# Performance work log

Measured on AMD Instinct MI355X. Metric: run time of the kernel, lower is better.

Reference implementation:

```python
import jax, jax.numpy as jnp
import numpy as np
from jax.lax.linalg import triangular_solve

B, T, D = 4, 2048, 1024
H, HD = 16, 64
K_OPS, R = 4, 48
POWER_K = 2
RIDGE_EPS = 1e-4
LN_EPS = 1e-5


def setup_inputs() -> dict:
    key = jax.random.key(0)
    ks = jax.random.split(key, 8)
    s = 1.0 / np.sqrt(D)
    return {
        "hidden_states": jax.random.normal(ks[0], (B, T, D), dtype=jnp.float32),
        "W_K_ops": jax.random.normal(ks[1], (K_OPS, D, H * R), dtype=jnp.float32) * s,
        "W_Q_ops": jax.random.normal(ks[2], (K_OPS, D, H * R), dtype=jnp.float32) * s,
        "W_V": jax.random.normal(ks[3], (D, H * HD), dtype=jnp.float32) * s,
        "W_O": jax.random.normal(ks[4], (H * HD, D), dtype=jnp.float32) * (1.0 / np.sqrt(H * HD)),
        "ln_gamma": jnp.ones((D,), dtype=jnp.float32),
        "ln_beta": jnp.zeros((D,), dtype=jnp.float32),
        "gate_alphas": jnp.zeros((K_OPS,), dtype=jnp.float32),
        "gate_alpha": jnp.zeros((1,), dtype=jnp.float32),
        "log_ridges": jnp.full((K_OPS,), np.log(RIDGE_EPS), dtype=jnp.float32),
        "log_gammas": jnp.zeros((K_OPS,), dtype=jnp.float32),
        "prefix_len": T // 2,
    }


def _layer_norm(x, g, b):
    mu = jnp.mean(x, axis=-1, keepdims=True)
    var = jnp.var(x, axis=-1, keepdims=True)
    return (x - mu) * jax.lax.rsqrt(var + LN_EPS) * g + b


def _solve_lower(L, rhs, transpose=False):
    # batched solve of L x = rhs (or L^T x = rhs), L lower-triangular [.., r, r]
    return triangular_solve(L, rhs, left_side=True, lower=True, transpose_a=transpose)


def reference(hidden_states, W_K_ops, W_Q_ops, W_V, W_O, ln_gamma, ln_beta,
              gate_alphas, gate_alpha, log_ridges, log_gammas, prefix_len):
    Bsz, Tlen, _ = hidden_states.shape
    pl = max(1, min(int(prefix_len), Tlen - 1))
    normed = _layer_norm(hidden_states, ln_gamma, ln_beta)
    # values: [B, H, T, HD]
    values = (normed @ W_V).reshape(Bsz, Tlen, H, HD).transpose(0, 2, 1, 3)
    eye_r = jnp.eye(R, dtype=hidden_states.dtype)
    acc = jnp.zeros((Bsz, H, Tlen, HD), dtype=hidden_states.dtype)
    for k in range(K_OPS):
        ridge = jnp.exp(log_ridges[k])
        gamma = jnp.exp(log_gammas[k])
        gate_k = jax.nn.sigmoid(gate_alphas[k])
        keys = (normed @ W_K_ops[k]).reshape(Bsz, Tlen, H, R).transpose(0, 2, 1, 3)    # [B,H,T,R]
        queries = (normed @ W_Q_ops[k]).reshape(Bsz, Tlen, H, R).transpose(0, 2, 1, 3)  # [B,H,T,R]
        pk = keys[:, :, :pl, :]   # prefix keys [B,H,pl,R]
        # Gram and cross-covariance (rank-R, batched over B*H)
        G = jnp.einsum('bhlr,bhls->bhrs', pk, pk) + ridge * eye_r
        M = jnp.einsum('bhlr,bhls->bhrs', pk[:, :, 1:, :], pk[:, :, :-1, :])
        Lc = jnp.linalg.cholesky(G)                         # [B,H,R,R] lower
        U = _solve_lower(Lc, M)
        V = _solve_lower(Lc, jnp.swapaxes(U, -1, -2))
        A_w = jnp.swapaxes(V, -1, -2)                       # Koopman operator [B,H,R,R]
        # spectral-norm scaling
        sigma_max = jnp.linalg.svd(A_w, compute_uv=False)[..., 0][..., None, None]
        sigma_max = jnp.maximum(sigma_max, 1e-8)
        scale = jnp.minimum(gamma, 1.0) / jnp.maximum(sigma_max, 1.0)
        A_w = A_w * scale
        # value readout B_v = C_v G^{-1}
        pv = values[:, :, :pl, :]
        C_v = jnp.einsum('bhld,bhlr->bhdr', pv, pk)          # [B,H,HD,R]
        Y_T = _solve_lower(Lc, jnp.swapaxes(C_v, -1, -2))
        Bv_T = _solve_lower(Lc, Y_T, transpose=True)
        B_v = jnp.swapaxes(Bv_T, -1, -2)                     # [B,H,HD,R]
        # whitened queries + power iteration
        q_t = jnp.swapaxes(queries, -1, -2)                  # [B,H,R,T]
        w_f = _solve_lower(Lc, q_t)
        for _ in range(POWER_K):
            w_f = A_w @ w_f
        z_hat = Lc @ w_f                                     # [B,H,R,T]
        out_k = jnp.swapaxes(B_v @ z_hat, -1, -2)            # [B,H,T,HD]
        acc = acc + gate_k * out_k
    out = acc.transpose(0, 2, 1, 3).reshape(Bsz, Tlen, H * HD) @ W_O
    return jax.nn.sigmoid(gate_alpha) * out
```

## Files before the change

kernel.cpp:

```cpp
#include <hip/hip_runtime.h>
#include <math.h>

typedef unsigned short u16;
typedef __attribute__((ext_vector_type(8))) short bf16x8;
typedef __attribute__((ext_vector_type(4))) float f32x4;

#define BSZ 4
#define TLEN 2048
#define DDIM 1024
#define NH 16
#define HDIM 64
#define NKOPS 4
#define RDIM 48
#define HR 768
#define HHD 1024
#define NALL 4096
#define LNEPS 1e-5f
#define GSPLIT 16
#define SST 52

#define AS1 __attribute__((address_space(1)))
#define AS3 __attribute__((address_space(3)))

static __device__ __forceinline__ void gload16(const u16* g, u16* l) {
    __builtin_amdgcn_global_load_lds((const AS1 unsigned int*)g, (AS3 unsigned int*)l, 16, 0, 0);
}

static __device__ __forceinline__ int clamp_pl(int p) {
    if (p < 1) p = 1;
    if (p > TLEN - 1) p = TLEN - 1;
    return p;
}

static __device__ __forceinline__ u16 f2bf(float x) {
    unsigned u = __float_as_uint(x);
    return (u16)((u + 0x7FFFu + ((u >> 16) & 1u)) >> 16);
}
static __device__ __forceinline__ float bf2f(u16 h) {
    return __uint_as_float(((unsigned)h) << 16);
}

static __device__ __forceinline__ float dot48(const float* __restrict__ a,
                                              const float* __restrict__ b) {
    float s0 = 0.f, s1 = 0.f, s2 = 0.f, s3 = 0.f;
#pragma unroll
    for (int m = 0; m < 12; ++m) {
        float4 av = *(const float4*)(a + m * 4);
        float4 bv = *(const float4*)(b + m * 4);
        s0 += av.x * bv.x; s1 += av.y * bv.y;
        s2 += av.z * bv.z; s3 += av.w * bv.w;
    }
    return (s0 + s1) + (s2 + s3);
}

static __device__ __forceinline__ void mm48_3x3(const float* __restrict__ Lb,
                                                const float* __restrict__ Rb,
                                                int i0, int j0, float acc[3][3]) {
#pragma unroll
    for (int r = 0; r < 3; ++r)
#pragma unroll
        for (int c = 0; c < 3; ++c) acc[r][c] = 0.f;
#pragma unroll 4
    for (int m = 0; m < 12; ++m) {
        float4 a0 = *(const float4*)(Lb + (i0 + 0) * SST + m * 4);
        float4 a1 = *(const float4*)(Lb + (i0 + 1) * SST + m * 4);
        float4 a2 = *(const float4*)(Lb + (i0 + 2) * SST + m * 4);
        float4 b0 = *(const float4*)(Rb + (j0 + 0) * SST + m * 4);
        float4 b1 = *(const float4*)(Rb + (j0 + 1) * SST + m * 4);
        float4 b2 = *(const float4*)(Rb + (j0 + 2) * SST + m * 4);
        acc[0][0] += a0.x * b0.x + a0.y * b0.y + a0.z * b0.z + a0.w * b0.w;
        acc[0][1] += a0.x * b1.x + a0.y * b1.y + a0.z * b1.z + a0.w * b1.w;
        acc[0][2] += a0.x * b2.x + a0.y * b2.y + a0.z * b2.z + a0.w * b2.w;
        acc[1][0] += a1.x * b0.x + a1.y * b0.y + a1.z * b0.z + a1.w * b0.w;
        acc[1][1] += a1.x * b1.x + a1.y * b1.y + a1.z * b1.z + a1.w * b1.w;
        acc[1][2] += a1.x * b2.x + a1.y * b2.y + a1.z * b2.z + a1.w * b2.w;
        acc[2][0] += a2.x * b0.x + a2.y * b0.y + a2.z * b0.z + a2.w * b0.w;
        acc[2][1] += a2.x * b1.x + a2.y * b1.y + a2.z * b1.z + a2.w * b1.w;
        acc[2][2] += a2.x * b2.x + a2.y * b2.y + a2.z * b2.z + a2.w * b2.w;
    }
}

#define WB() __builtin_amdgcn_wave_barrier()

__global__ __launch_bounds__(256) void ln_kernel(const float* __restrict__ hs,
                                                 const float* __restrict__ g,
                                                 const float* __restrict__ b,
                                                 u16* __restrict__ nh,
                                                 u16* __restrict__ nl)
{
    int row = blockIdx.x;
    int tid = threadIdx.x;
    const float* x = hs + (size_t)row * DDIM;
    float4 v = ((const float4*)x)[tid];
    float s  = v.x + v.y + v.z + v.w;
    float ss = v.x*v.x + v.y*v.y + v.z*v.z + v.w*v.w;
    for (int off = 32; off > 0; off >>= 1) {
        s  += __shfl_down(s, off);
        ss += __shfl_down(ss, off);
    }
    __shared__ float rs[4], rss[4], st[2];
    int wid = tid >> 6, lane = tid & 63;
    if (lane == 0) { rs[wid] = s; rss[wid] = ss; }
    __syncthreads();
    if (tid == 0) {
        float S  = rs[0] + rs[1] + rs[2] + rs[3];
        float SS = rss[0] + rss[1] + rss[2] + rss[3];
        float mu = S / (float)DDIM;
        float var = SS / (float)DDIM - mu * mu;
        st[0] = mu;
        st[1] = rsqrtf(var + LNEPS);
    }
    __syncthreads();
    float mu = st[0], rstd = st[1];
    float4 gv = ((const float4*)g)[tid];
    float4 bv = ((const float4*)b)[tid];
    float o[4];
    o[0] = (v.x - mu) * rstd * gv.x + bv.x;
    o[1] = (v.y - mu) * rstd * gv.y + bv.y;
    o[2] = (v.z - mu) * rstd * gv.z + bv.z;
    o[3] = (v.w - mu) * rstd * gv.w + bv.w;
    u16 h[4], l[4];
#pragma unroll
    for (int i = 0; i < 4; ++i) {
        h[i] = f2bf(o[i]);
        l[i] = f2bf(o[i] - bf2f(h[i]));
    }
    uint2 ph, pl2;
    ph.x = (unsigned)h[0] | ((unsigned)h[1] << 16);
    ph.y = (unsigned)h[2] | ((unsigned)h[3] << 16);
    pl2.x = (unsigned)l[0] | ((unsigned)l[1] << 16);
    pl2.y = (unsigned)l[2] | ((unsigned)l[3] << 16);
    *(uint2*)(nh + (size_t)row * DDIM + tid * 4) = ph;
    *(uint2*)(nl + (size_t)row * DDIM + tid * 4) = pl2;
}

__global__ __launch_bounds__(256) void transcvt(const float* __restrict__ in,
                                                u16* __restrict__ oh,
                                                u16* __restrict__ ol,
                                                int R, int C)
{
    __shared__ float t[32][33];
    int bx = blockIdx.x, by = blockIdx.y;
    int tx = threadIdx.x & 31, ty = threadIdx.x >> 5;
#pragma unroll
    for (int j = 0; j < 4; ++j)
        t[ty + j * 8][tx] = in[(size_t)(by * 32 + ty + j * 8) * C + bx * 32 + tx];
    __syncthreads();
#pragma unroll
    for (int j = 0; j < 4; ++j) {
        float v = t[tx][ty + j * 8];
        u16 h = f2bf(v);
        size_t o = (size_t)(bx * 32 + ty + j * 8) * R + by * 32 + tx;
        oh[o] = h;
        ol[o] = f2bf(v - bf2f(h));
    }
}

__global__ __launch_bounds__(256) void transcvt_wk(const float* __restrict__ WK,
                                                   u16* __restrict__ oh,
                                                   u16* __restrict__ ol)
{
    __shared__ float t[32][33];
    int bx = blockIdx.x, by = blockIdx.y, k = blockIdx.z;
    const float* in = WK + (size_t)k * DDIM * HR;
    u16* ohk = oh + (size_t)k * (HR * DDIM);
    u16* olk = ol + (size_t)k * (HR * DDIM);
    int tx = threadIdx.x & 31, ty = threadIdx.x >> 5;
#pragma unroll
    for (int j = 0; j < 4; ++j)
        t[ty + j * 8][tx] = in[(size_t)(by * 32 + ty + j * 8) * HR + bx * 32 + tx];
    __syncthreads();
#pragma unroll
    for (int j = 0; j < 4; ++j) {
        float v = t[tx][ty + j * 8];
        u16 h = f2bf(v);
        size_t o = (size_t)(bx * 32 + ty + j * 8) * DDIM + by * 32 + tx;
        ohk[o] = h;
        olk[o] = f2bf(v - bf2f(h));
    }
}

template<int OMODE>
__global__ __launch_bounds__(256) void gemm_mfma(
    const u16* __restrict__ Ah, const u16* __restrict__ Al, long sAz,
    const u16* __restrict__ Bth, const u16* __restrict__ Btl, long sBz,
    float* __restrict__ C, u16* __restrict__ Oh, u16* __restrict__ Ol, long sCz,
    int M, int N, int K,
    const int* __restrict__ pl_ptr, const float* __restrict__ gate_ptr)
{
    int z = blockIdx.z;
    int m0 = blockIdx.y * 128, n0 = blockIdx.x * 128;
    if (pl_ptr) {
        int p = clamp_pl(pl_ptr[0]);
        if (m0 >= (p < M ? p : M)) return;
    }
    Ah  += (size_t)z * sAz;  Al  += (size_t)z * sAz;
    Bth += (size_t)z * sBz;  Btl += (size_t)z * sBz;

    __shared__ u16 As[2][128][32];
    __shared__ u16 Bs[2][128][32];

    int tid = threadIdx.x;
    int wid = tid >> 6, ln = tid & 63;
    int wm = (wid >> 1) * 64, wn = (wid & 1) * 64;
    int r16 = ln & 15, kg = ln >> 4;

    int rb = wid * 32;
    int lr = ln >> 2;
    int sl = ln & 3;
    int koff = (sl ^ (((rb + lr) >> 1) & 3)) * 8;

    const u16* gA0h = Ah  + (size_t)(m0 + rb + lr) * K + koff;
    const u16* gA1h = gA0h + (size_t)16 * K;
    const u16* gA0l = Al  + (size_t)(m0 + rb + lr) * K + koff;
    const u16* gA1l = gA0l + (size_t)16 * K;
    const u16* gB0h = Bth + (size_t)(n0 + rb + lr) * K + koff;
    const u16* gB1h = gB0h + (size_t)16 * K;
    const u16* gB0l = Btl + (size_t)(n0 + rb + lr) * K + koff;
    const u16* gB1l = gB0l + (size_t)16 * K;

    u16* lA0h = &As[0][rb][0];      u16* lA1h = &As[0][rb + 16][0];
    u16* lA0l = &As[1][rb][0];      u16* lA1l = &As[1][rb + 16][0];
    u16* lB0h = &Bs[0][rb][0];      u16* lB1h = &Bs[0][rb + 16][0];
    u16* lB0l = &Bs[1][rb][0];      u16* lB1l = &Bs[1][rb + 16][0];

    f32x4 acc[4][4];
#pragma unroll
    for (int mt = 0; mt < 4; ++mt)
#pragma unroll
        for (int nt = 0; nt < 4; ++nt)
            acc[mt][nt] = (f32x4){0.f, 0.f, 0.f, 0.f};

    for (int k0 = 0; k0 < K; k0 += 32) {
        __syncthreads();
        gload16(gA0h, lA0h);  gload16(gA1h, lA1h);
        gload16(gA0l, lA0l);  gload16(gA1l, lA1l);
        gload16(gB0h, lB0h);  gload16(gB1h, lB1h);
        gload16(gB0l, lB0l);  gload16(gB1l, lB1l);
        gA0h += 32; gA1h += 32; gA0l += 32; gA1l += 32;
        gB0h += 32; gB1h += 32; gB0l += 32; gB1l += 32;
        __syncthreads();

        bf16x8 bhf[4], blf[4];
#pragma unroll
        for (int nt = 0; nt < 4; ++nt) {
            int r = wn + nt * 16 + r16;
            int s = (kg ^ ((r >> 1) & 3)) * 8;
            bhf[nt] = *(const bf16x8*)&Bs[0][r][s];
            blf[nt] = *(const bf16x8*)&Bs[1][r][s];
        }
#pragma unroll
        for (int mt = 0; mt < 4; ++mt) {
            int r = wm + mt * 16 + r16;
            int s = (kg ^ ((r >> 1) & 3)) * 8;
            bf16x8 ah = *(const bf16x8*)&As[0][r][s];
            bf16x8 al = *(const bf16x8*)&As[1][r][s];
#pragma unroll
            for (int nt = 0; nt < 4; ++nt) {
                acc[mt][nt] = __builtin_amdgcn_mfma_f32_16x16x32_bf16(ah, bhf[nt], acc[mt][nt], 0, 0, 0);
                acc[mt][nt] = __builtin_amdgcn_mfma_f32_16x16x32_bf16(ah, blf[nt], acc[mt][nt], 0, 0, 0);
                acc[mt][nt] = __builtin_amdgcn_mfma_f32_16x16x32_bf16(al, bhf[nt], acc[mt][nt], 0, 0, 0);
            }
        }
    }

    int orow0 = m0 + wm + kg * 4;
    int ocol0 = n0 + wn + r16;
    if (OMODE == 0) {
        float scale = 1.0f;
        if (gate_ptr) scale = 1.0f / (1.0f + expf(-gate_ptr[0]));
        float* Cz = C + (size_t)z * sCz;
#pragma unroll
        for (int mt = 0; mt < 4; ++mt)
#pragma unroll
            for (int nt = 0; nt < 4; ++nt)
#pragma unroll
                for (int j = 0; j < 4; ++j)
                    Cz[(size_t)(orow0 + mt * 16 + j) * N + ocol0 + nt * 16] = acc[mt][nt][j] * scale;
    } else {
        u16* Ohz = Oh + (size_t)z * sCz;
        u16* Olz = Ol + (size_t)z * sCz;
#pragma unroll
        for (int mt = 0; mt < 4; ++mt)
#pragma unroll
            for (int nt = 0; nt < 4; ++nt)
#pragma unroll
                for (int j = 0; j < 4; ++j) {
                    float v = acc[mt][nt][j];
                    u16 h = f2bf(v);
                    size_t o = (size_t)(orow0 + mt * 16 + j) * N + ocol0 + nt * 16;
                    Ohz[o] = h;
                    Olz[o] = f2bf(v - bf2f(h));
                }
    }
}

__global__ __launch_bounds__(256) void gram_kernel(const float* __restrict__ Kp,
                                                   const float* __restrict__ Vp,
                                                   float* __restrict__ Gpart,
                                                   float* __restrict__ Mpart,
                                                   float* __restrict__ Cpart,
                                                   const int* __restrict__ pl_ptr)
{
    int h = blockIdx.x, b = blockIdx.y, sp = blockIdx.z;
    int pl = clamp_pl(pl_ptr[0]);
    __shared__ float pks[65][48];
    __shared__ float pvs[64][64];
    int tid = threadIdx.x;
    int tx = tid & 15, ty = tid >> 4;
    float gacc[3][3] = {}, macc[3][3] = {}, cacc[4][3] = {};
    const float* Kbase = Kp + (size_t)b * TLEN * HR + h * RDIM;
    const float* Vbase = Vp + (size_t)b * TLEN * HHD + h * HDIM;
    const float4 z4 = make_float4(0.f, 0.f, 0.f, 0.f);

    for (int c0 = sp * 64; c0 < pl; c0 += GSPLIT * 64) {
        for (int idx = tid; idx < 65 * 12; idx += 256) {
            int rr = idx / 12, c4 = idx % 12;
            int tg = c0 + rr;
            *(float4*)&pks[rr][c4 * 4] =
                (tg < pl) ? *(const float4*)&Kbase[(size_t)tg * HR + c4 * 4] : z4;
        }
        for (int idx = tid; idx < 64 * 16; idx += 256) {
            int rr = idx >> 4, c4 = idx & 15;
            int tg = c0 + rr;
            *(float4*)&pvs[rr][c4 * 4] =
                (tg < pl) ? *(const float4*)&Vbase[(size_t)tg * HHD + c4 * 4] : z4;
        }
        __syncthreads();
        float cura[3], curb[3];
#pragma unroll
        for (int i = 0; i < 3; ++i) {
            cura[i] = pks[0][tx * 3 + i];
            curb[i] = pks[0][ty * 3 + i];
        }
#pragma unroll 2
        for (int l = 0; l < 64; ++l) {
            float nxta[3], nxtb[3];
#pragma unroll
            for (int i = 0; i < 3; ++i) {
                nxta[i] = pks[l + 1][tx * 3 + i];
                nxtb[i] = pks[l + 1][ty * 3 + i];
            }
            float4 v4 = *(const float4*)&pvs[l][ty * 4];
            float vv[4] = { v4.x, v4.y, v4.z, v4.w };
#pragma unroll
            for (int i = 0; i < 3; ++i)
#pragma unroll
                for (int j = 0; j < 3; ++j) {
                    gacc[i][j] += cura[i] * curb[j];
                    macc[i][j] += nxta[i] * curb[j];
                }
#pragma unroll
            for (int j = 0; j < 4; ++j)
#pragma unroll
                for (int i = 0; i < 3; ++i)
                    cacc[j][i] += vv[j] * cura[i];
#pragma unroll
            for (int i = 0; i < 3; ++i) { cura[i] = nxta[i]; curb[i] = nxtb[i]; }
        }
        __syncthreads();
    }
    size_t pbase = (size_t)sp * (BSZ * NH) + b * NH + h;
    float* Gp = Gpart + pbase * 2304;
    float* Mp = Mpart + pbase * 2304;
    float* Cp = Cpart + pbase * 3072;
#pragma unroll
    for (int i = 0; i < 3; ++i)
#pragma unroll
        for (int j = 0; j < 3; ++j) {
            Gp[(tx * 3 + i) * 48 + (ty * 3 + j)] = gacc[i][j];
            Mp[(tx * 3 + i) * 48 + (ty * 3 + j)] = macc[i][j];
        }
#pragma unroll
    for (int j = 0; j < 4; ++j)
#pragma unroll
        for (int i = 0; i < 3; ++i)
            Cp[(ty * 4 + j) * 48 + (tx * 3 + i)] = cacc[j][i];
}

__global__ __launch_bounds__(256) void gram_all(const float* __restrict__ Call,
                                                float* __restrict__ Gpart,
                                                float* __restrict__ Mpart,
                                                float* __restrict__ Cpart,
                                                const int* __restrict__ pl_ptr)
{
    int h = blockIdx.x, b = blockIdx.y, zz = blockIdx.z;
    int k = zz >> 2, sp = zz & 3;
    int pl = clamp_pl(pl_ptr[0]);
    __shared__ float pks[65][48];
    __shared__ float pvs[64][64];
    int tid = threadIdx.x;
    int tx = tid & 15, ty = tid >> 4;
    float gacc[3][3] = {}, macc[3][3] = {}, cacc[4][3] = {};
    const float* Kbase = Call + (size_t)b * TLEN * NALL + (HHD + k * HR) + h * RDIM;
    const float* Vbase = Call + (size_t)b * TLEN * NALL + h * HDIM;
    const float4 z4 = make_float4(0.f, 0.f, 0.f, 0.f);

    for (int c0 = sp * 64; c0 < pl; c0 += 4 * 64) {
        for (int idx = tid; idx < 65 * 12; idx += 256) {
            int rr = idx / 12, c4 = idx % 12;
            int tg = c0 + rr;
            *(float4*)&pks[rr][c4 * 4] =
                (tg < pl) ? *(const float4*)&Kbase[(size_t)tg * NALL + c4 * 4] : z4;
        }
        for (int idx = tid; idx < 64 * 16; idx += 256) {
            int rr = idx >> 4, c4 = idx & 15;
            int tg = c0 + rr;
            *(float4*)&pvs[rr][c4 * 4] =
                (tg < pl) ? *(const float4*)&Vbase[(size_t)tg * NALL + c4 * 4] : z4;
        }
        __syncthreads();
        float cura[3], curb[3];
#pragma unroll
        for (int i = 0; i < 3; ++i) {
            cura[i] = pks[0][tx * 3 + i];
            curb[i] = pks[0][ty * 3 + i];
        }
#pragma unroll 2
        for (int l = 0; l < 64; ++l) {
            float nxta[3], nxtb[3];
#pragma unroll
            for (int i = 0; i < 3; ++i) {
                nxta[i] = pks[l + 1][tx * 3 + i];
                nxtb[i] = pks[l + 1][ty * 3 + i];
            }
            float4 v4 = *(const float4*)&pvs[l][ty * 4];
            float vv[4] = { v4.x, v4.y, v4.z, v4.w };
#pragma unroll
            for (int i = 0; i < 3; ++i)
#pragma unroll
                for (int j = 0; j < 3; ++j) {
                    gacc[i][j] += cura[i] * curb[j];
                    macc[i][j] += nxta[i] * curb[j];
                }
#pragma unroll
            for (int j = 0; j < 4; ++j)
#pragma unroll
                for (int i = 0; i < 3; ++i)
                    cacc[j][i] += vv[j] * cura[i];
#pragma unroll
            for (int i = 0; i < 3; ++i) { cura[i] = nxta[i]; curb[i] = nxtb[i]; }
        }
        __syncthreads();
    }
    size_t pbase = (size_t)zz * (BSZ * NH) + b * NH + h;
    float* Gp = Gpart + pbase * 2304;
    float* Mp = Mpart + pbase * 2304;
    float* Cp = Cpart + pbase * 3072;
#pragma unroll
    for (int i = 0; i < 3; ++i)
#pragma unroll
        for (int j = 0; j < 3; ++j) {
            Gp[(tx * 3 + i) * 48 + (ty * 3 + j)] = gacc[i][j];
            Mp[(tx * 3 + i) * 48 + (ty * 3 + j)] = macc[i][j];
        }
#pragma unroll
    for (int j = 0; j < 4; ++j)
#pragma unroll
        for (int i = 0; i < 3; ++i)
            Cp[(ty * 4 + j) * 48 + (tx * 3 + i)] = cacc[j][i];
}

__global__ __launch_bounds__(256) void gram_reduce(const float* __restrict__ Gpart,
                                                   const float* __restrict__ Mpart,
                                                   const float* __restrict__ Cpart,
                                                   float* __restrict__ Gb,
                                                   float* __restrict__ Mb,
                                                   float* __restrict__ Cb,
                                                   int k)
{
    int p = blockIdx.x;
    size_t ob = ((size_t)k * (BSZ * NH) + p);
    for (int idx = threadIdx.x; idx < 2304; idx += 256) {
        float sg = 0.f, sm = 0.f;
#pragma unroll
        for (int sp = 0; sp < GSPLIT; ++sp) {
            size_t pb = ((size_t)sp * (BSZ * NH) + p);
            sg += Gpart[pb * 2304 + idx];
            sm += Mpart[pb * 2304 + idx];
        }
        Gb[ob * 2304 + idx] = sg;
        Mb[ob * 2304 + idx] = sm;
    }
    for (int idx = threadIdx.x; idx < 3072; idx += 256) {
        float sc = 0.f;
#pragma unroll
        for (int sp = 0; sp < GSPLIT; ++sp)
            sc += Cpart[((size_t)sp * (BSZ * NH) + p) * 3072 + idx];
        Cb[ob * 3072 + idx] = sc;
    }
}

__global__ __launch_bounds__(256) void gram_reduce_all(const float* __restrict__ Gpart,
                                                       const float* __restrict__ Mpart,
                                                       const float* __restrict__ Cpart,
                                                       float* __restrict__ Gb,
                                                       float* __restrict__ Mb,
                                                       float* __restrict__ Cb)
{
    int blk = blockIdx.x;
    int k = blk >> 6, p = blk & 63;
    size_t ob = (size_t)blk;
    for (int idx = threadIdx.x; idx < 2304; idx += 256) {
        float sg = 0.f, sm = 0.f;
#pragma unroll
        for (int sp = 0; sp < 4; ++sp) {
            size_t pb = ((size_t)(k * 4 + sp) * (BSZ * NH) + p);
            sg += Gpart[pb * 2304 + idx];
            sm += Mpart[pb * 2304 + idx];
        }
        Gb[ob * 2304 + idx] = sg;
        Mb[ob * 2304 + idx] = sm;
    }
    for (int idx = threadIdx.x; idx < 3072; idx += 256) {
        float sc = 0.f;
#pragma unroll
        for (int sp = 0; sp < 4; ++sp)
            sc += Cpart[((size_t)(k * 4 + sp) * (BSZ * NH) + p) * 3072 + idx];
        Cb[ob * 3072 + idx] = sc;
    }
}

__global__ __launch_bounds__(256) void solver_kernel(const float* __restrict__ Gb,
                                                     const float* __restrict__ Mb,
                                                     const float* __restrict__ Cb,
                                                     float* __restrict__ Fb,
                                                     const float* __restrict__ log_ridges,
                                                     const float* __restrict__ log_gammas)
{
    int blk = blockIdx.x;
    int k = blk / (BSZ * NH);
    int tid = threadIdx.x;
    int ti = tid >> 4, tj = tid & 15;
    int i0 = ti * 3, j0 = tj * 3;

    __shared__ float A [48 * SST];
    __shared__ float Hs[48 * SST];
    __shared__ float Mm[48 * SST];
    __shared__ float Pm[48 * SST];
    __shared__ float Pt[48 * SST];
    __shared__ float pvb[4][SST];

    size_t base = (size_t)blk;
    const float* Gp = Gb + base * 2304;
    const float* Mp = Mb + base * 2304;
    const float* Cp = Cb + base * 3072;
    float ridge = expf(log_ridges[k]);

    for (int idx = tid; idx < 2304; idx += 256) {
        int i = idx / 48, j = idx % 48;
        A [i * SST + j] = Gp[idx] + ((i == j) ? ridge : 0.f);
        Hs[i * SST + j] = (i == j) ? 1.f : 0.f;
        Mm[i * SST + j] = Mp[idx];
    }
    __syncthreads();

    for (int p = 0; p < 48; ++p) {
        int p4 = p >> 2;
        float pr = 1.0f / fmaxf(A[p * SST + p], 1e-30f);
        int c4a = p4 + 1;
        int nA4 = 11 - p4;
        int nb  = 3 - (p & 3);
        for (int q = tid; q < 576; q += 256) {
            int i = q / 12, c = q % 12;
            if (i == p) continue;
            float f = A[i * SST + p] * pr;
            if (c < nA4) {
                int c4 = c4a + c;
                float4 prw = *(const float4*)&A[p * SST + c4 * 4];
                float4* d = (float4*)&A[i * SST + c4 * 4];
                float4 v = *d;
                v.x -= f * prw.x; v.y -= f * prw.y;
                v.z -= f * prw.z; v.w -= f * prw.w;
                *d = v;
            } else {
                int c4 = c - nA4;
                float4 prw = *(const float4*)&Hs[p * SST + c4 * 4];
                float4* d = (float4*)&Hs[i * SST + c4 * 4];
                float4 v = *d;
                v.x -= f * prw.x; v.y -= f * prw.y;
                v.z -= f * prw.z; v.w -= f * prw.w;
                *d = v;
            }
        }
        if (nb) {
            for (int i = tid; i < 48; i += 256) {
                if (i == p) continue;
                float f = A[i * SST + p] * pr;
                for (int c = p + 1; c < 4 * c4a; ++c)
                    A[i * SST + c] -= f * A[p * SST + c];
            }
        }
        __syncthreads();
    }
    for (int idx = tid; idx < 2304; idx += 256) {
        int i = idx / 48, j = idx % 48;
        Hs[i * SST + j] /= fmaxf(A[i * SST + i], 1e-30f);
    }
    __syncthreads();
    for (int idx = tid; idx < 2304; idx += 256) {
        int i = idx / 48, j = idx % 48;
        A[j * SST + i] = Mm[i * SST + j];
    }
    __syncthreads();
    {
        float acc[3][3];
        mm48_3x3(Hs, A, i0, j0, acc);
#pragma unroll
        for (int r = 0; r < 3; ++r)
#pragma unroll
            for (int c = 0; c < 3; ++c) {
                Pm[(i0 + r) * SST + j0 + c] = acc[r][c];
                Pt[(j0 + c) * SST + i0 + r] = acc[r][c];
            }
    }
    __syncthreads();
    {
        float acc[3][3];
        mm48_3x3(Hs, Mm, i0, j0, acc);
        __syncthreads();
#pragma unroll
        for (int r = 0; r < 3; ++r)
#pragma unroll
            for (int c = 0; c < 3; ++c)
                A[(i0 + r) * SST + j0 + c] = acc[r][c];
    }
    __syncthreads();
    {
        float acc[3][3];
        mm48_3x3(A, Pt, i0, j0, acc);
        __syncthreads();
#pragma unroll
        for (int r = 0; r < 3; ++r)
#pragma unroll
            for (int c = 0; c < 3; ++c) {
                Mm[(i0 + r) * SST + j0 + c] = acc[r][c];
                A [(j0 + c) * SST + i0 + r] = acc[r][c];
            }
    }
    __syncthreads();
    {
        float acc[3][3];
        mm48_3x3(Mm, A, i0, j0, acc);
#pragma unroll
        for (int r = 0; r < 3; ++r)
#pragma unroll
            for (int c = 0; c < 3; ++c)
                Pt[(i0 + r) * SST + j0 + c] = acc[r][c];
    }
    __syncthreads();
    for (int idx = tid; idx < 2304; idx += 256) {
        int i = idx / 48, j = idx % 48;
        A[j * SST + i] = Pt[i * SST + j];
    }
    __syncthreads();
    {
        float acc[3][3];
        mm48_3x3(Pt, A, i0, j0, acc);
        __syncthreads();
#pragma unroll
        for (int r = 0; r < 3; ++r)
#pragma unroll
            for (int c = 0; c < 3; ++c)
                Mm[(i0 + r) * SST + j0 + c] = acc[r][c];
    }
    __syncthreads();

    int ln = tid & 63, w = tid >> 6;
    float* pv = pvb[w];
    if (ln < 48) pv[ln] = ((float)((ln * 2654435761u) & 0xFFFF)) / 65536.0f + 0.5f;
    WB();
    float lam = 0.f;
    for (int it = 0; it < 25; ++it) {
        float z = 0.f;
        if (ln < 48) z = dot48(&Mm[ln * SST], pv);
        if (it == 24) {
            float nn = z * z;
            for (int off = 1; off < 64; off <<= 1) nn += __shfl_xor(nn, off);
            lam = sqrtf(nn);
            break;
        }
        if ((it & 1) == 1) {
            float nn = z * z;
            for (int off = 1; off < 64; off <<= 1) nn += __shfl_xor(nn, off);
            z *= rsqrtf(fmaxf(nn, 1e-30f));
        }
        WB();
        if (ln < 48) pv[ln] = z;
        WB();
    }
    float sigma = sqrtf(sqrtf(sqrtf(fmaxf(lam, 0.f))));
    float gamma = expf(log_gammas[k]);
    float scl = fminf(gamma, 1.f) / fmaxf(fmaxf(sigma, 1e-8f), 1.f);
    float s2 = scl * scl;

    {
        float acc[3][3];
        mm48_3x3(Pm, Hs, i0, j0, acc);
        __syncthreads();
#pragma unroll
        for (int r = 0; r < 3; ++r)
#pragma unroll
            for (int c = 0; c < 3; ++c)
                A[(j0 + c) * SST + i0 + r] = acc[r][c];
    }
    __syncthreads();
    {
        float acc[3][3];
        mm48_3x3(Pm, A, i0, j0, acc);
        __syncthreads();
#pragma unroll
        for (int r = 0; r < 3; ++r)
#pragma unroll
            for (int c = 0; c < 3; ++c)
                Pt[(j0 + c) * SST + i0 + r] = s2 * acc[r][c];
    }
    __syncthreads();
    for (int idx = tid; idx < 3072; idx += 256) {
        int row = idx / 48, col = idx % 48;
        float v = Cp[idx];
        if (row < 48) Mm[row * SST + col] = v;
        else          A [(row - 48) * SST + col] = v;
    }
    __syncthreads();
    {
        int fi0 = ti * 4, fj0 = tj * 3;
        const float* crow0 = (fi0 < 48) ? &Mm[fi0 * SST] : &A[(fi0 - 48) * SST];
        float acc[4][3];
#pragma unroll
        for (int r = 0; r < 4; ++r)
#pragma unroll
            for (int c = 0; c < 3; ++c) acc[r][c] = 0.f;
#pragma unroll 4
        for (int m = 0; m < 12; ++m) {
            float4 a0 = *(const float4*)(crow0 + 0 * SST + m * 4);
            float4 a1 = *(const float4*)(crow0 + 1 * SST + m * 4);
            float4 a2 = *(const float4*)(crow0 + 2 * SST + m * 4);
            float4 a3 = *(const float4*)(crow0 + 3 * SST + m * 4);
            float4 b0 = *(const float4*)(&Pt[(fj0 + 0) * SST] + m * 4);
            float4 b1 = *(const float4*)(&Pt[(fj0 + 1) * SST] + m * 4);
            float4 b2 = *(const float4*)(&Pt[(fj0 + 2) * SST] + m * 4);
            acc[0][0] += a0.x*b0.x + a0.y*b0.y + a0.z*b0.z + a0.w*b0.w;
            acc[0][1] += a0.x*b1.x + a0.y*b1.y + a0.z*b1.z + a0.w*b1.w;
            acc[0][2] += a0.x*b2.x + a0.y*b2.y + a0.z*b2.z + a0.w*b2.w;
            acc[1][0] += a1.x*b0.x + a1.y*b0.y + a1.z*b0.z + a1.w*b0.w;
            acc[1][1] += a1.x*b1.x + a1.y*b1.y + a1.z*b1.z + a1.w*b1.w;
            acc[1][2] += a1.x*b2.x + a1.y*b2.y + a1.z*b2.z + a1.w*b2.w;
            acc[2][0] += a2.x*b0.x + a2.y*b0.y + a2.z*b0.z + a2.w*b0.w;
            acc[2][1] += a2.x*b1.x + a2.y*b1.y + a2.z*b1.z + a2.w*b1.w;
            acc[2][2] += a2.x*b2.x + a2.y*b2.y + a2.z*b2.z + a2.w*b2.w;
            acc[3][0] += a3.x*b0.x + a3.y*b0.y + a3.z*b0.z + a3.w*b0.w;
            acc[3][1] += a3.x*b1.x + a3.y*b1.y + a3.z*b1.z + a3.w*b1.w;
            acc[3][2] += a3.x*b2.x + a3.y*b2.y + a3.z*b2.z + a3.w*b2.w;
        }
#pragma unroll
        for (int r = 0; r < 4; ++r)
#pragma unroll
            for (int c = 0; c < 3; ++c)
                Fb[base * 3072 + (size_t)(fi0 + r) * 48 + fj0 + c] = acc[r][c];
    }
}

__global__ __launch_bounds__(256) void wcmb_kernel(const float* __restrict__ WQ,
                                                   const float* __restrict__ Fb,
                                                   const float* __restrict__ gate_alphas,
                                                   u16* __restrict__ Wh,
                                                   u16* __restrict__ Wl)
{
    int dt = blockIdx.x;
    int h = blockIdx.y, b = blockIdx.z;
    __shared__ float wq[64][49];
    __shared__ float fs[64][49];
    int tid = threadIdx.x;
    int tx = tid & 15, ty = tid >> 4;
    float acc[4][4] = {};
    for (int k = 0; k < NKOPS; ++k) {
        float gate = 1.0f / (1.0f + expf(-gate_alphas[k]));
        for (int idx = tid; idx < 64 * 48; idx += 256) {
            int rr = idx / 48, cc = idx % 48;
            wq[rr][cc] = WQ[((size_t)k * DDIM + dt * 64 + rr) * HR + h * RDIM + cc];
            fs[rr][cc] = gate * Fb[(((size_t)k * BSZ + b) * NH + h) * 3072 + idx];
        }
        __syncthreads();
        for (int r = 0; r < 48; ++r) {
            float a[4], bb[4];
#pragma unroll
            for (int i = 0; i < 4; ++i) { a[i] = wq[tx * 4 + i][r]; bb[i] = fs[ty * 4 + i][r]; }
#pragma unroll
            for (int i = 0; i < 4; ++i)
#pragma unroll
                for (int j = 0; j < 4; ++j)
                    acc[i][j] += a[i] * bb[j];
        }
        __syncthreads();
    }
#pragma unroll
    for (int i = 0; i < 4; ++i)
#pragma unroll
        for (int j = 0; j < 4; ++j) {
            size_t o = ((size_t)b * DDIM + dt * 64 + tx * 4 + i) * HHD + h * HDIM + ty * 4 + j;
            float v = acc[i][j];
            u16 hh = f2bf(v);
            Wh[o] = hh;
            Wl[o] = f2bf(v - bf2f(hh));
        }
}

extern "C" void kernel_launch(void* const* d_in, const int* in_sizes, int n_in,
                              void* d_out, int out_size, void* d_ws, size_t ws_size,
                              hipStream_t stream)
{
    const float* hs          = (const float*)d_in[0];
    const float* WK          = (const float*)d_in[1];
    const float* WQ          = (const float*)d_in[2];
    const float* WV          = (const float*)d_in[3];
    const float* WO          = (const float*)d_in[4];
    const float* ln_g        = (const float*)d_in[5];
    const float* ln_b        = (const float*)d_in[6];
    const float* gate_alphas = (const float*)d_in[7];
    const float* gate_alpha  = (const float*)d_in[8];
    const float* log_ridges  = (const float*)d_in[9];
    const float* log_gammas  = (const float*)d_in[10];
    const int*   pl_ptr      = (const int*)d_in[11];
    float* out = (float*)d_out;
    float* wsf = (float*)d_ws;

    float* Gpart = out;
    float* Mpart = out + 2359296;
    float* Cpart = out + 4718592;

    const size_t BIG_NEED = (size_t)(12582912 + 33554432) * 4;

    if (ws_size >= BIG_NEED) {
        u16* n_hi    = (u16*)(wsf + 0);
        u16* n_lo    = (u16*)(wsf + 4194304);
        u16* Wall_h  = (u16*)(wsf + 8388608);
        u16* Wall_l  = (u16*)(wsf + 10485760);
        u16* WVt_h   = Wall_h;
        u16* WVt_l   = Wall_l;
        u16* WKt_ah  = Wall_h + (size_t)HHD * DDIM;
        u16* WKt_al  = Wall_l + (size_t)HHD * DDIM;
        float* Call  = wsf + 12582912;
        float* Gb    = Call;
        float* Mb    = Call + 589824;
        float* Cb    = Call + 1179648;
        u16* WOt_h   = (u16*)(Call + 2097152);
        u16* WOt_l   = (u16*)(Call + 2621440);
        float* Fb    = Call + 3145728;
        u16* Wcmb_h  = (u16*)(Call + 4194304);
        u16* Wcmb_l  = (u16*)(Call + 6291456);
        u16* Wfint_h = (u16*)(Call + 8388608);
        u16* Wfint_l = (u16*)(Call + 10485760);

        ln_kernel<<<BSZ * TLEN, 256, 0, stream>>>(hs, ln_g, ln_b, n_hi, n_lo);
        transcvt<<<dim3(HHD / 32, DDIM / 32), 256, 0, stream>>>(WV, WVt_h, WVt_l, DDIM, HHD);
        transcvt_wk<<<dim3(HR / 32, DDIM / 32, NKOPS), 256, 0, stream>>>(WK, WKt_ah, WKt_al);

        gemm_mfma<0><<<dim3(NALL / 128, TLEN / 128, BSZ), 256, 0, stream>>>(
            n_hi, n_lo, (long)TLEN * DDIM, Wall_h, Wall_l, 0,
            Call, nullptr, nullptr, (long)TLEN * NALL,
            TLEN, NALL, DDIM, pl_ptr, nullptr);

        gram_all<<<dim3(NH, BSZ, 16), 256, 0, stream>>>(Call, Gpart, Mpart, Cpart, pl_ptr);
        gram_reduce_all<<<NKOPS * BSZ * NH, 256, 0, stream>>>(Gpart, Mpart, Cpart, Gb, Mb, Cb);

        transcvt<<<dim3(DDIM / 32, HHD / 32), 256, 0, stream>>>(WO, WOt_h, WOt_l, HHD, DDIM);

        solver_kernel<<<NKOPS * BSZ * NH, 256, 0, stream>>>(Gb, Mb, Cb, Fb, log_ridges, log_gammas);
        wcmb_kernel<<<dim3(DDIM / 64, NH, BSZ), 256, 0, stream>>>(WQ, Fb, gate_alphas, Wcmb_h, Wcmb_l);

        gemm_mfma<1><<<dim3(DDIM / 128, DDIM / 128, BSZ), 256, 0, stream>>>(
            WOt_h, WOt_l, 0, Wcmb_h, Wcmb_l, (long)DDIM * HHD,
            nullptr, Wfint_h, Wfint_l, (long)DDIM * DDIM,
            DDIM, DDIM, HHD, nullptr, nullptr);

        gemm_mfma<0><<<dim3(DDIM / 128, TLEN / 128, BSZ), 256, 0, stream>>>(
            n_hi, n_lo, (long)TLEN * DDIM, Wfint_h, Wfint_l, (long)DDIM * DDIM,
            out, nullptr, nullptr, (long)TLEN * DDIM,
            TLEN, DDIM, DDIM, nullptr, gate_alpha);
        return;
    }

    u16* n_hi    = (u16*)(wsf + 0);
    u16* n_lo    = (u16*)(wsf + 4194304);
    u16* WVt_h   = (u16*)(wsf + 8388608);
    u16* WVt_l   = (u16*)(wsf + 8912896);
    u16* WKt_ah  = (u16*)(wsf + 9437184);
    u16* WKt_al  = (u16*)(wsf + 11010048);
    float* Vp    = wsf + 12582912;
    float* Kp    = wsf + 20971520;
    float* Gb    = wsf + 27262976;
    float* Mb    = wsf + 27852800;
    float* Cb    = wsf + 28442624;
    u16* Wcmb_h  = (u16*)Vp;
    u16* Wcmb_l  = (u16*)(Vp + 2097152);
    u16* Wfint_h = (u16*)(Vp + 4194304);
    u16* Wfint_l = (u16*)(Vp + 6291456);
    u16* WOt_h   = (u16*)Kp;
    u16* WOt_l   = (u16*)(Kp + 524288);
    float* Fb    = Kp + 1048576;

    ln_kernel<<<BSZ * TLEN, 256, 0, stream>>>(hs, ln_g, ln_b, n_hi, n_lo);
    transcvt_wk<<<dim3(HR / 32, DDIM / 32, NKOPS), 256, 0, stream>>>(WK, WKt_ah, WKt_al);
    transcvt<<<dim3(HHD / 32, DDIM / 32), 256, 0, stream>>>(WV, WVt_h, WVt_l, DDIM, HHD);

    gemm_mfma<0><<<dim3(HHD / 128, TLEN / 128, BSZ), 256, 0, stream>>>(
        n_hi, n_lo, (long)TLEN * DDIM, WVt_h, WVt_l, 0,
        Vp, nullptr, nullptr, (long)TLEN * HHD,
        TLEN, HHD, DDIM, pl_ptr, nullptr);

    for (int k = 0; k < NKOPS; ++k) {
        gemm_mfma<0><<<dim3(HR / 128, TLEN / 128, BSZ), 256, 0, stream>>>(
            n_hi, n_lo, (long)TLEN * DDIM,
            WKt_ah + (size_t)k * (HR * DDIM), WKt_al + (size_t)k * (HR * DDIM), 0,
            Kp, nullptr, nullptr, (long)TLEN * HR,
            TLEN, HR, DDIM, pl_ptr, nullptr);
        gram_kernel<<<dim3(NH, BSZ, GSPLIT), 256, 0, stream>>>(Kp, Vp, Gpart, Mpart, Cpart, pl_ptr);
        gram_reduce<<<BSZ * NH, 256, 0, stream>>>(Gpart, Mpart, Cpart, Gb, Mb, Cb, k);
    }

    transcvt<<<dim3(DDIM / 32, HHD / 32), 256, 0, stream>>>(WO, WOt_h, WOt_l, HHD, DDIM);

    solver_kernel<<<NKOPS * BSZ * NH, 256, 0, stream>>>(Gb, Mb, Cb, Fb, log_ridges, log_gammas);
    wcmb_kernel<<<dim3(DDIM / 64, NH, BSZ), 256, 0, stream>>>(WQ, Fb, gate_alphas, Wcmb_h, Wcmb_l);

    gemm_mfma<1><<<dim3(DDIM / 128, DDIM / 128, BSZ), 256, 0, stream>>>(
        WOt_h, WOt_l, 0, Wcmb_h, Wcmb_l, (long)DDIM * HHD,
        nullptr, Wfint_h, Wfint_l, (long)DDIM * DDIM,
        DDIM, DDIM, HHD, nullptr, nullptr);

    gemm_mfma<0><<<dim3(DDIM / 128, TLEN / 128, BSZ), 256, 0, stream>>>(
        n_hi, n_lo, (long)TLEN * DDIM, Wfint_h, Wfint_l, (long)DDIM * DDIM,
        out, nullptr, nullptr, (long)TLEN * DDIM,
        TLEN, DDIM, DDIM, nullptr, gate_alpha);
}
```

Measured before the change: 460.4 us.

## Write projection GEMM output head-blocked and fold gram reduction into solver

The fused V/K projection GEMM now scatters its output into per-head contiguous layouts ([B,H,T,64] for values, [B,K,H,T,48] for keys), so gram_blk reads compact rows instead of striding over 4096-wide rows. The separate gram_reduce_all kernel is removed, and the solver sums the split partials directly when it loads G, M and C. This cuts one launch and one intermediate round trip and improves locality in the gram loads. In exchange the GEMM epilogue does strided scalar stores with per-column index arithmetic, and every solver block repeats the partial-sum reads.

```diff
diff --git a/kernel.cpp b/kernel.cpp
--- a/kernel.cpp
+++ b/kernel.cpp
@@ -184,7 +184,7 @@
 __global__ __launch_bounds__(256) void gemm_mfma(
     const u16* __restrict__ Ah, const u16* __restrict__ Al, long sAz,
     const u16* __restrict__ Bth, const u16* __restrict__ Btl, long sBz,
-    float* __restrict__ C, u16* __restrict__ Oh, u16* __restrict__ Ol, long sCz,
+    float* __restrict__ C, float* __restrict__ C2, u16* __restrict__ Oh, u16* __restrict__ Ol, long sCz,
     int M, int N, int K,
     const int* __restrict__ pl_ptr, const float* __restrict__ gate_ptr)
 {
@@ -277,7 +277,7 @@
 #pragma unroll
                 for (int j = 0; j < 4; ++j)
                     Cz[(size_t)(orow0 + mt * 16 + j) * N + ocol0 + nt * 16] = acc[mt][nt][j] * scale;
-    } else {
+    } else if (OMODE == 1) {
         u16* Ohz = Oh + (size_t)z * sCz;
         u16* Olz = Ol + (size_t)z * sCz;
 #pragma unroll
@@ -292,6 +292,32 @@
                     Ohz[o] = h;
                     Olz[o] = f2bf(v - bf2f(h));
                 }
+    } else {
+#pragma unroll
+        for (int nt = 0; nt < 4; ++nt) {
+            int col = ocol0 + nt * 16;
+            if (col < HHD) {
+                int h = col >> 6, d = col & 63;
+                float* dst = C + (((size_t)z * NH + h) * TLEN) * 64 + d;
+#pragma unroll
+                for (int mt = 0; mt < 4; ++mt)
+#pragma unroll
+                    for (int j = 0; j < 4; ++j)
+                        dst[(size_t)(orow0 + mt * 16 + j) * 64] = acc[mt][nt][j];
+            } else {
+                int c = col - HHD;
+                int k = c / HR;
+                int rr = c - k * HR;
+                int h = rr / RDIM;
+                int r = rr - h * RDIM;
+                float* dst = C2 + ((((size_t)z * NKOPS + k) * NH + h) * TLEN) * 48 + r;
+#pragma unroll
+                for (int mt = 0; mt < 4; ++mt)
+#pragma unroll
+                    for (int j = 0; j < 4; ++j)
+                        dst[(size_t)(orow0 + mt * 16 + j) * 48] = acc[mt][nt][j];
+            }
+        }
     }
 }
 
@@ -378,7 +404,8 @@
             Cp[(ty * 4 + j) * 48 + (tx * 3 + i)] = cacc[j][i];
 }
 
-__global__ __launch_bounds__(256) void gram_all(const float* __restrict__ Call,
+__global__ __launch_bounds__(256) void gram_blk(const float* __restrict__ Vp2,
+                                                const float* __restrict__ Kp2,
                                                 float* __restrict__ Gpart,
                                                 float* __restrict__ Mpart,
                                                 float* __restrict__ Cpart,
@@ -392,8 +419,8 @@
     int tid = threadIdx.x;
     int tx = tid & 15, ty = tid >> 4;
     float gacc[3][3] = {}, macc[3][3] = {}, cacc[4][3] = {};
-    const float* Kbase = Call + (size_t)b * TLEN * NALL + (HHD + k * HR) + h * RDIM;
-    const float* Vbase = Call + (size_t)b * TLEN * NALL + h * HDIM;
+    const float* Kbase = Kp2 + ((((size_t)b * NKOPS + k) * NH + h) * TLEN) * 48;
+    const float* Vbase = Vp2 + (((size_t)b * NH + h) * TLEN) * 64;
     const float4 z4 = make_float4(0.f, 0.f, 0.f, 0.f);
 
     for (int c0 = sp * 64; c0 < pl; c0 += 4 * 64) {
@@ -401,13 +428,13 @@
             int rr = idx / 12, c4 = idx % 12;
             int tg = c0 + rr;
             *(float4*)&pks[rr][c4 * 4] =
-                (tg < pl) ? *(const float4*)&Kbase[(size_t)tg * NALL + c4 * 4] : z4;
+                (tg < pl) ? *(const float4*)&Kbase[(size_t)tg * 48 + c4 * 4] : z4;
         }
         for (int idx = tid; idx < 64 * 16; idx += 256) {
             int rr = idx >> 4, c4 = idx & 15;
             int tg = c0 + rr;
             *(float4*)&pvs[rr][c4 * 4] =
-                (tg < pl) ? *(const float4*)&Vbase[(size_t)tg * NALL + c4 * 4] : z4;
+                (tg < pl) ? *(const float4*)&Vbase[(size_t)tg * 64 + c4 * 4] : z4;
         }
         __syncthreads();
         float cura[3], curb[3];
@@ -491,45 +518,17 @@
     }
 }
 
-__global__ __launch_bounds__(256) void gram_reduce_all(const float* __restrict__ Gpart,
-                                                       const float* __restrict__ Mpart,
-                                                       const float* __restrict__ Cpart,
-                                                       float* __restrict__ Gb,
-                                                       float* __restrict__ Mb,
-                                                       float* __restrict__ Cb)
-{
-    int blk = blockIdx.x;
-    int k = blk >> 6, p = blk & 63;
-    size_t ob = (size_t)blk;
-    for (int idx = threadIdx.x; idx < 2304; idx += 256) {
-        float sg = 0.f, sm = 0.f;
-#pragma unroll
-        for (int sp = 0; sp < 4; ++sp) {
-            size_t pb = ((size_t)(k * 4 + sp) * (BSZ * NH) + p);
-            sg += Gpart[pb * 2304 + idx];
-            sm += Mpart[pb * 2304 + idx];
-        }
-        Gb[ob * 2304 + idx] = sg;
-        Mb[ob * 2304 + idx] = sm;
-    }
-    for (int idx = threadIdx.x; idx < 3072; idx += 256) {
-        float sc = 0.f;
-#pragma unroll
-        for (int sp = 0; sp < 4; ++sp)
-            sc += Cpart[((size_t)(k * 4 + sp) * (BSZ * NH) + p) * 3072 + idx];
-        Cb[ob * 3072 + idx] = sc;
-    }
-}
-
-__global__ __launch_bounds__(256) void solver_kernel(const float* __restrict__ Gb,
-                                                     const float* __restrict__ Mb,
-                                                     const float* __restrict__ Cb,
+__global__ __launch_bounds__(256) void solver_kernel(const float* __restrict__ Gpart,
+                                                     const float* __restrict__ Mpart,
+                                                     const float* __restrict__ Cpart,
+                                                     int nsum,
                                                      float* __restrict__ Fb,
                                                      const float* __restrict__ log_ridges,
                                                      const float* __restrict__ log_gammas)
 {
     int blk = blockIdx.x;
     int k = blk / (BSZ * NH);
+    int p64 = blk - k * (BSZ * NH);
     int tid = threadIdx.x;
     int ti = tid >> 4, tj = tid & 15;
     int i0 = ti * 3, j0 = tj * 3;
@@ -542,16 +541,19 @@
     __shared__ float pvb[4][SST];
 
     size_t base = (size_t)blk;
-    const float* Gp = Gb + base * 2304;
-    const float* Mp = Mb + base * 2304;
-    const float* Cp = Cb + base * 3072;
     float ridge = expf(log_ridges[k]);
 
     for (int idx = tid; idx < 2304; idx += 256) {
         int i = idx / 48, j = idx % 48;
-        A [i * SST + j] = Gp[idx] + ((i == j) ? ridge : 0.f);
+        float sg = 0.f, sm = 0.f;
+        for (int sp = 0; sp < nsum; ++sp) {
+            size_t pb = ((size_t)(k * nsum + sp) * (BSZ * NH) + p64);
+            sg += Gpart[pb * 2304 + idx];
+            sm += Mpart[pb * 2304 + idx];
+        }
+        A [i * SST + j] = sg + ((i == j) ? ridge : 0.f);
         Hs[i * SST + j] = (i == j) ? 1.f : 0.f;
-        Mm[i * SST + j] = Mp[idx];
+        Mm[i * SST + j] = sm;
     }
     __syncthreads();
 
@@ -718,9 +720,11 @@
     __syncthreads();
     for (int idx = tid; idx < 3072; idx += 256) {
         int row = idx / 48, col = idx % 48;
-        float v = Cp[idx];
-        if (row < 48) Mm[row * SST + col] = v;
-        else          A [(row - 48) * SST + col] = v;
+        float sc = 0.f;
+        for (int sp = 0; sp < nsum; ++sp)
+            sc += Cpart[((size_t)(k * nsum + sp) * (BSZ * NH) + p64) * 3072 + idx];
+        if (row < 48) Mm[row * SST + col] = sc;
+        else          A [(row - 48) * SST + col] = sc;
     }
     __syncthreads();
     {
@@ -825,9 +829,9 @@
     float* out = (float*)d_out;
     float* wsf = (float*)d_ws;
 
-    float* Gpart = out;
-    float* Mpart = out + 2359296;
-    float* Cpart = out + 4718592;
+    float* GpartO = out;
+    float* MpartO = out + 2359296;
+    float* CpartO = out + 4718592;
 
     const size_t BIG_NEED = (size_t)(12582912 + 33554432) * 4;
 
@@ -840,43 +844,41 @@
         u16* WVt_l   = Wall_l;
         u16* WKt_ah  = Wall_h + (size_t)HHD * DDIM;
         u16* WKt_al  = Wall_l + (size_t)HHD * DDIM;
-        float* Call  = wsf + 12582912;
-        float* Gb    = Call;
-        float* Mb    = Call + 589824;
-        float* Cb    = Call + 1179648;
-        u16* WOt_h   = (u16*)(Call + 2097152);
-        u16* WOt_l   = (u16*)(Call + 2621440);
-        float* Fb    = Call + 3145728;
-        u16* Wcmb_h  = (u16*)(Call + 4194304);
-        u16* Wcmb_l  = (u16*)(Call + 6291456);
-        u16* Wfint_h = (u16*)(Call + 8388608);
-        u16* Wfint_l = (u16*)(Call + 10485760);
+        float* Vp2   = wsf + 12582912;
+        float* Kp2   = wsf + 20971520;
+        u16* WOt_h   = (u16*)(wsf + 12582912);
+        u16* WOt_l   = (u16*)(wsf + 13107200);
+        float* Fb    = wsf + 13631488;
+        u16* Wcmb_h  = (u16*)(wsf + 14417920);
+        u16* Wcmb_l  = (u16*)(wsf + 16515072);
+        u16* Wfint_h = (u16*)(wsf + 18612224);
+        u16* Wfint_l = (u16*)(wsf + 20709376);
 
         ln_kernel<<<BSZ * TLEN, 256, 0, stream>>>(hs, ln_g, ln_b, n_hi, n_lo);
         transcvt<<<dim3(HHD / 32, DDIM / 32), 256, 0, stream>>>(WV, WVt_h, WVt_l, DDIM, HHD);
         transcvt_wk<<<dim3(HR / 32, DDIM / 32, NKOPS), 256, 0, stream>>>(WK, WKt_ah, WKt_al);
 
-        gemm_mfma<0><<<dim3(NALL / 128, TLEN / 128, BSZ), 256, 0, stream>>>(
+        gemm_mfma<2><<<dim3(NALL / 128, TLEN / 128, BSZ), 256, 0, stream>>>(
             n_hi, n_lo, (long)TLEN * DDIM, Wall_h, Wall_l, 0,
-            Call, nullptr, nullptr, (long)TLEN * NALL,
+            Vp2, Kp2, nullptr, nullptr, 0,
             TLEN, NALL, DDIM, pl_ptr, nullptr);
 
-        gram_all<<<dim3(NH, BSZ, 16), 256, 0, stream>>>(Call, Gpart, Mpart, Cpart, pl_ptr);
-        gram_reduce_all<<<NKOPS * BSZ * NH, 256, 0, stream>>>(Gpart, Mpart, Cpart, Gb, Mb, Cb);
+        gram_blk<<<dim3(NH, BSZ, 16), 256, 0, stream>>>(Vp2, Kp2, GpartO, MpartO, CpartO, pl_ptr);
 
         transcvt<<<dim3(DDIM / 32, HHD / 32), 256, 0, stream>>>(WO, WOt_h, WOt_l, HHD, DDIM);
 
-        solver_kernel<<<NKOPS * BSZ * NH, 256, 0, stream>>>(Gb, Mb, Cb, Fb, log_ridges, log_gammas);
+        solver_kernel<<<NKOPS * BSZ * NH, 256, 0, stream>>>(
+            GpartO, MpartO, CpartO, 4, Fb, log_ridges, log_gammas);
         wcmb_kernel<<<dim3(DDIM / 64, NH, BSZ), 256, 0, stream>>>(WQ, Fb, gate_alphas, Wcmb_h, Wcmb_l);
 
         gemm_mfma<1><<<dim3(DDIM / 128, DDIM / 128, BSZ), 256, 0, stream>>>(
             WOt_h, WOt_l, 0, Wcmb_h, Wcmb_l, (long)DDIM * HHD,
-            nullptr, Wfint_h, Wfint_l, (long)DDIM * DDIM,
+            nullptr, nullptr, Wfint_h, Wfint_l, (long)DDIM * DDIM,
             DDIM, DDIM, HHD, nullptr, nullptr);
 
         gemm_mfma<0><<<dim3(DDIM / 128, TLEN / 128, BSZ), 256, 0, stream>>>(
             n_hi, n_lo, (long)TLEN * DDIM, Wfint_h, Wfint_l, (long)DDIM * DDIM,
-            out, nullptr, nullptr, (long)TLEN * DDIM,
+            out, nullptr, nullptr, nullptr, (long)TLEN * DDIM,
             TLEN, DDIM, DDIM, nullptr, gate_alpha);
         return;
     }
@@ -906,31 +908,31 @@
 
     gemm_mfma<0><<<dim3(HHD / 128, TLEN / 128, BSZ), 256, 0, stream>>>(
         n_hi, n_lo, (long)TLEN * DDIM, WVt_h, WVt_l, 0,
-        Vp, nullptr, nullptr, (long)TLEN * HHD,
+        Vp, nullptr, nullptr, nullptr, (long)TLEN * HHD,
         TLEN, HHD, DDIM, pl_ptr, nullptr);
 
     for (int k = 0; k < NKOPS; ++k) {
         gemm_mfma<0><<<dim3(HR / 128, TLEN / 128, BSZ), 256, 0, stream>>>(
             n_hi, n_lo, (long)TLEN * DDIM,
             WKt_ah + (size_t)k * (HR * DDIM), WKt_al + (size_t)k * (HR * DDIM), 0,
-            Kp, nullptr, nullptr, (long)TLEN * HR,
+            Kp, nullptr, nullptr, nullptr, (long)TLEN * HR,
             TLEN, HR, DDIM, pl_ptr, nullptr);
-        gram_kernel<<<dim3(NH, BSZ, GSPLIT), 256, 0, stream>>>(Kp, Vp, Gpart, Mpart, Cpart, pl_ptr);
-        gram_reduce<<<BSZ * NH, 256, 0, stream>>>(Gpart, Mpart, Cpart, Gb, Mb, Cb, k);
+        gram_kernel<<<dim3(NH, BSZ, GSPLIT), 256, 0, stream>>>(Kp, Vp, GpartO, MpartO, CpartO, pl_ptr);
+        gram_reduce<<<BSZ * NH, 256, 0, stream>>>(GpartO, MpartO, CpartO, Gb, Mb, Cb, k);
     }
 
     transcvt<<<dim3(DDIM / 32, HHD / 32), 256, 0, stream>>>(WO, WOt_h, WOt_l, HHD, DDIM);
 
-    solver_kernel<<<NKOPS * BSZ * NH, 256, 0, stream>>>(Gb, Mb, Cb, Fb, log_ridges, log_gammas);
+    solver_kernel<<<NKOPS * BSZ * NH, 256, 0, stream>>>(Gb, Mb, Cb, 1, Fb, log_ridges, log_gammas);
     wcmb_kernel<<<dim3(DDIM / 64, NH, BSZ), 256, 0, stream>>>(WQ, Fb, gate_alphas, Wcmb_h, Wcmb_l);
 
     gemm_mfma<1><<<dim3(DDIM / 128, DDIM / 128, BSZ), 256, 0, stream>>>(
         WOt_h, WOt_l, 0, Wcmb_h, Wcmb_l, (long)DDIM * HHD,
-        nullptr, Wfint_h, Wfint_l, (long)DDIM * DDIM,
+        nullptr, nullptr, Wfint_h, Wfint_l, (long)DDIM * DDIM,
         DDIM, DDIM, HHD, nullptr, nullptr);
 
     gemm_mfma<0><<<dim3(DDIM / 128, TLEN / 128, BSZ), 256, 0, stream>>>(
         n_hi, n_lo, (long)TLEN * DDIM, Wfint_h, Wfint_l, (long)DDIM * DDIM,
-        out, nullptr, nullptr, (long)TLEN * DDIM,
+        out, nullptr, nullptr, nullptr, (long)TLEN * DDIM,
         TLEN, DDIM, DDIM, nullptr, gate_alpha);
 }
```

Measured after the change: 452.7 us. About the same (-1.7%).
